# Kernel optimization log

Hardware: AMD Instinct MI355X
Metric: run time of the kernel (lower is better)

## Reference

```python
import jax, jax.numpy as jnp
import numpy as np
import math

B, P = 64, 2048
E_DRUG, E_PATH = 512, 512
ATTN_DIM, H, DEPTH = 1024, 8, 1
HD = ATTN_DIM // (2 * H)          # head_dim = 64
SCALING = HD ** (-0.5)
LAMBDA_INIT = 0.8 - 0.6 * math.exp(-0.3 * DEPTH)
EPS_SM = 1e-20
EPS_RMS = 1e-5


def stable_softmax(x, eps=EPS_SM):
    x = x.astype(jnp.float32)
    x = x - jnp.max(x, axis=-1, keepdims=True)
    ex = jnp.exp(x)
    return ex / (jnp.sum(ex, axis=-1, keepdims=True) + eps)


def setup_inputs() -> dict:
    key = jax.random.key(0)
    ks = jax.random.split(key, 11)
    d = 2 * H * HD  # = ATTN_DIM
    return {
        "query": jax.random.normal(ks[0], (B, 1, E_DRUG), jnp.float32),
        "key": jax.random.normal(ks[1], (B, P, E_PATH), jnp.float32),
        # Linear weights stored [in, out] (transpose of torch storage; same math)
        "Wq": jax.random.normal(ks[2], (E_DRUG, d), jnp.float32) * 0.02,
        "Wk": jax.random.normal(ks[3], (E_PATH, d), jnp.float32) * 0.02,
        "Wv": jax.random.normal(ks[4], (E_PATH, d), jnp.float32) * 0.02,
        "Wo": jax.random.normal(ks[5], (d, E_DRUG), jnp.float32) * 0.02,
        "lambda_q1": jax.random.normal(ks[6], (HD,), jnp.float32) * 0.1,
        "lambda_k1": jax.random.normal(ks[7], (HD,), jnp.float32) * 0.1,
        "lambda_q2": jax.random.normal(ks[8], (HD,), jnp.float32) * 0.1,
        "lambda_k2": jax.random.normal(ks[9], (HD,), jnp.float32) * 0.1,
        "rms_weight": jnp.ones((2 * HD,), jnp.float32),
    }


def reference(query, key, Wq, Wk, Wv, Wo,
              lambda_q1, lambda_k1, lambda_q2, lambda_k2, rms_weight):
    # Q: [B,1,H,2,HD] -> [B,H,2,1,HD]; K,V: [B,P,H,2,HD] -> [B,H,2,P,HD]
    Q = (query @ Wq).reshape(B, 1, H, 2, HD).transpose(0, 2, 3, 1, 4) * SCALING
    K = (key @ Wk).reshape(B, P, H, 2, HD).transpose(0, 2, 3, 1, 4)
    V = (key @ Wv).reshape(B, P, H, 2, HD)

    # scores: [B,H,2,1,P]
    scores = jnp.einsum('bhsqd,bhskd->bhsqk', Q, K)
    scores = stable_softmax(scores)

    lam1 = jnp.exp(jnp.sum(lambda_q1 * lambda_k1))
    lam2 = jnp.exp(jnp.sum(lambda_q2 * lambda_k2))
    lam = lam1 - lam2 + LAMBDA_INIT

    diff_attn = scores[:, :, 0] - lam * scores[:, :, 1]  # [B,H,1,P]

    V_cat = V.transpose(0, 2, 1, 3, 4).reshape(B, H, P, 2 * HD)  # [B,H,P,2HD]
    out = jnp.einsum('bhqp,bhpd->bhqd', diff_attn, V_cat)        # [B,H,1,2HD]

    # RMSNorm over last dim, affine
    var = jnp.mean(out * out, axis=-1, keepdims=True)
    out = out * jax.lax.rsqrt(var + EPS_RMS) * rms_weight
    out = out * (1.0 - LAMBDA_INIT)

    out = out.transpose(0, 2, 1, 3).reshape(B, 1, 2 * H * HD)
    out = out @ Wo  # [B,1,E_DRUG]
    return out, diff_attn
```

## Files before the change

### kernel.cpp

```cpp
#include <hip/hip_runtime.h>
#include <hip/hip_bf16.h>
#include <math.h>

#define B_ 64
#define P_ 2048
#define E_ 512
#define H_ 8
#define D_ 1024
#define NC_ 32
#define NG_ 4
#define SMEM_FUSED (65536 + 8704 + 2304 + 64 + 64)

#define BAR() do { __builtin_amdgcn_sched_barrier(0); \
                   asm volatile("s_waitcnt lgkmcnt(0)"); \
                   __builtin_amdgcn_s_barrier(); \
                   __builtin_amdgcn_sched_barrier(0); } while (0)

#define KXOR(row) ((((row) & 7) << 3) ^ (((row) & 8) << 1) ^ (((row) & 16) >> 1))

static constexpr float SCALING_C = 0.125f;
static constexpr float LAMBDA_INIT_C = 0.35550906759096966f;

typedef float f32x4 __attribute__((ext_vector_type(4)));
typedef float f32x2 __attribute__((ext_vector_type(2)));
typedef short bf16x8 __attribute__((ext_vector_type(8)));
typedef short bf16x4 __attribute__((ext_vector_type(4)));

static __device__ __forceinline__ short f2bf(float f) {
    __hip_bfloat16 h = __float2bfloat16(f);
    return __builtin_bit_cast(short, h);
}

__global__ __launch_bounds__(256) void k_qproj(const float* __restrict__ query,
                                               const float* __restrict__ Wq,
                                               const float* __restrict__ Wk,
                                               unsigned short* __restrict__ qkfrag) {
    int x = blockIdx.x, b = blockIdx.y, t = threadIdx.x;
    __shared__ float q[E_];
    __shared__ float qh[256];
    q[t] = query[b * E_ + t];
    q[t + 256] = query[b * E_ + t + 256];
    __syncthreads();
    {
        int j = x * 256 + t;
        const float* w = Wq + j;
        float s[8] = {0.f,0.f,0.f,0.f,0.f,0.f,0.f,0.f};
        #pragma unroll 4
        for (int e = 0; e < E_; e += 8) {
            #pragma unroll
            for (int k = 0; k < 8; ++k) s[k] += q[e + k] * w[(long)(e + k) * D_];
        }
        qh[t] = (((s[0]+s[1])+(s[2]+s[3])) + ((s[4]+s[5])+(s[6]+s[7]))) * SCALING_C;
    }
    __syncthreads();
    int hs_loc = t >> 6, l = t & 63;
    int hs = x * 4 + hs_loc;
    int e0 = l * 8;
    const float* qp = qh + hs_loc * 64;
    float acc[8];
    #pragma unroll
    for (int jj = 0; jj < 8; ++jj) {
        const f32x4* w = (const f32x4*)(Wk + (long)(e0 + jj) * D_ + hs * 64);
        float s = 0.f;
        #pragma unroll
        for (int d4 = 0; d4 < 16; ++d4) {
            f32x4 wv = w[d4];
            s += qp[d4 * 4 + 0] * wv[0] + qp[d4 * 4 + 1] * wv[1]
               + qp[d4 * 4 + 2] * wv[2] + qp[d4 * 4 + 3] * wv[3];
        }
        acc[jj] = s;
    }
    bf16x8 v;
    #pragma unroll
    for (int jj = 0; jj < 8; ++jj) v[jj] = f2bf(acc[jj]);
    *(bf16x8*)(qkfrag + (((long)b * 16 + (l >> 2)) * 64 + (l & 3) * 16 + hs) * 8) = v;
}

__global__ __launch_bounds__(512, 2) void k_fusedp(const float* __restrict__ key,
                                                   const unsigned short* __restrict__ qkfrag,
                                                   float* __restrict__ wexp,
                                                   float* __restrict__ ms, float* __restrict__ zs,
                                                   float* __restrict__ apart) {
    extern __shared__ __align__(16) char smem[];
    unsigned short* kswz = (unsigned short*)smem;
    float* scr           = (float*)(smem + 65536);
    unsigned short* wbf  = (unsigned short*)(smem + 74240);
    float* fac_l         = (float*)(smem + 76544);
    float* mrun_l        = (float*)(smem + 76608);

    int pcg = blockIdx.x, b = blockIdx.y;
    int t = threadIdx.x, wv = t >> 6, l = t & 63;
    int rt = wv >> 1, eh = wv & 1;
    int prow = rt * 16 + (l & 15);
    int xorv = KXOR(prow);
    int hi = t >> 7;
    int col4 = t & 127;

    if (t < 16) mrun_l[t] = -3.0e38f;

    bf16x8 qfr[8];
    {
        const bf16x8* qf = (const bf16x8*)(qkfrag + (long)b * 16 * 64 * 8);
        #pragma unroll
        for (int s = 0; s < 8; ++s) qfr[s] = qf[(eh * 8 + s) * 64 + l];
    }

    const float* kchunk = key + ((long)b * P_ + pcg * 512) * E_;

    f32x4 x[16];
    #pragma unroll
    for (int r = 0; r < 16; ++r)
        x[r] = *(const f32x4*)(kchunk + (long)(r * 512 + t) * 4);

    f32x4 accp[4];
    #pragma unroll
    for (int i = 0; i < 4; ++i) accp[i] = {0.f, 0.f, 0.f, 0.f};

    for (int c = 0; c < 8; ++c) {
        #pragma unroll
        for (int r = 0; r < 16; ++r) {
            int row = 4 * r + hi;
            int xr = KXOR(row);
            bf16x4 wb;
            wb[0] = f2bf(x[r][0]); wb[1] = f2bf(x[r][1]);
            wb[2] = f2bf(x[r][2]); wb[3] = f2bf(x[r][3]);
            *(bf16x4*)(kswz + row * 512 + ((col4 * 4) ^ xr)) = wb;
        }
        if (c < 7) {
            const float* kn = kchunk + (long)(c + 1) * 64 * E_;
            #pragma unroll
            for (int r = 0; r < 16; ++r)
                x[r] = *(const f32x4*)(kn + (long)(r * 512 + t) * 4);
        }
        BAR();

        {
            f32x4 acc = {0.f, 0.f, 0.f, 0.f};
            #pragma unroll
            for (int s = 0; s < 8; ++s) {
                int e8 = eh * 256 + (l >> 4) * 8 + s * 32;
                bf16x8 a = *(const bf16x8*)(kswz + prow * 512 + (e8 ^ xorv));
                acc = __builtin_amdgcn_mfma_f32_16x16x32_bf16(a, qfr[s], acc, 0, 0, 0);
            }
            #pragma unroll
            for (int r = 0; r < 4; ++r)
                scr[eh * 1088 + (l & 15) * 68 + rt * 16 + (l >> 4) * 4 + r] = acc[r];
        }
        BAR();

        {
            int hs = t >> 5, i = t & 31;
            const float* s0p = scr + hs * 68 + i * 2;
            const float* s1p = s0p + 1088;
            float v0 = s0p[0] + s1p[0];
            float v1 = s0p[1] + s1p[1];
            float m = fmaxf(v0, v1);
            #pragma unroll
            for (int o = 16; o > 0; o >>= 1) m = fmaxf(m, __shfl_xor(m, o));
            float e0v = expf(v0 - m), e1v = expf(v1 - m);
            float z = e0v + e1v;
            #pragma unroll
            for (int o = 16; o > 0; o >>= 1) z += __shfl_xor(z, o);
            float mold = mrun_l[hs];
            float mnew = fmaxf(mold, m);
            float wsc = expf(m - mnew);
            if (i == 0) {
                mrun_l[hs] = mnew;
                fac_l[hs] = expf(mold - mnew);
                ms[((long)(pcg * 8 + c) * B_ + b) * 16 + hs] = m;
                zs[((long)(pcg * 8 + c) * B_ + b) * 16 + hs] = z;
            }
            f32x2 wv2; wv2[0] = e0v; wv2[1] = e1v;
            *(f32x2*)(wexp + ((long)b * 16 + hs) * P_ + pcg * 512 + c * 64 + i * 2) = wv2;
            unsigned lo = (unsigned short)f2bf(e0v * wsc);
            unsigned hi2 = (unsigned short)f2bf(e1v * wsc);
            *(unsigned*)(wbf + hs * 72 + i * 2) = lo | (hi2 << 16);
        }
        BAR();

        {
            f32x4 frv;
            frv[0] = fac_l[(l >> 4) * 4 + 0];
            frv[1] = fac_l[(l >> 4) * 4 + 1];
            frv[2] = fac_l[(l >> 4) * 4 + 2];
            frv[3] = fac_l[(l >> 4) * 4 + 3];
            const unsigned short* wrow = wbf + (l & 15) * 72;
            bf16x8 af0 = *(const bf16x8*)(wrow + (l >> 4) * 8);
            bf16x8 af1 = *(const bf16x8*)(wrow + 32 + (l >> 4) * 8);
            #pragma unroll
            for (int tile = 0; tile < 4; ++tile) {
                accp[tile] = accp[tile] * frv;
                int e = wv * 64 + tile * 16 + (l & 15);
                #pragma unroll
                for (int ks = 0; ks < 2; ++ks) {
                    int pbase = ks * 32 + (l >> 4) * 8;
                    bf16x8 af = ks ? af1 : af0;
                    int xc = ((pbase & 8) << 1) ^ ((pbase & 16) >> 1);
                    bf16x8 bfv;
                    #pragma unroll
                    for (int j = 0; j < 8; ++j)
                        bfv[j] = (short)kswz[(pbase + j) * 512 + (e ^ (j << 3) ^ xc)];
                    accp[tile] = __builtin_amdgcn_mfma_f32_16x16x32_bf16(af, bfv, accp[tile], 0, 0, 0);
                }
            }
        }
        BAR();
    }

    {
        long abase = ((long)pcg * B_ + b) * 16 * E_;
        #pragma unroll
        for (int tile = 0; tile < 4; ++tile) {
            int e = wv * 64 + tile * 16 + (l & 15);
            #pragma unroll
            for (int r = 0; r < 4; ++r)
                apart[abase + (long)((l >> 4) * 4 + r) * E_ + e] = accp[tile][r];
        }
    }
}

__global__ __launch_bounds__(256) void k_comb(const float* __restrict__ wexp,
                                              const float* __restrict__ ms, const float* __restrict__ zs,
                                              const float* __restrict__ apart,
                                              const float* __restrict__ lq1, const float* __restrict__ lk1,
                                              const float* __restrict__ lq2, const float* __restrict__ lk2,
                                              const float* __restrict__ Wv, const float* __restrict__ rmsw,
                                              float* __restrict__ out1, float* __restrict__ on) {
    int h = blockIdx.x, b = blockIdx.y, t = threadIdx.x;
    __shared__ float lam_s;
    __shared__ float mc0s[NC_], mc1s[NC_], zc0s[NC_], zc1s[NC_];
    __shared__ float c0s[NC_], c1s[NC_];
    __shared__ float attk[E_];
    __shared__ float onred[2][128];
    __shared__ float red[4];
    int hs0 = 2 * h, hs1 = 2 * h + 1;
    if (t < 64) {
        float v1 = lq1[t] * lk1[t];
        float v2 = lq2[t] * lk2[t];
        #pragma unroll
        for (int o = 32; o > 0; o >>= 1) { v1 += __shfl_xor(v1, o); v2 += __shfl_xor(v2, o); }
        if (t == 0) lam_s = expf(v1) - expf(v2) + LAMBDA_INIT_C;
    }
    if (t >= 64 && t < 64 + NC_) {
        int c = t - 64;
        mc0s[c] = ms[((long)c * B_ + b) * 16 + hs0];
        mc1s[c] = ms[((long)c * B_ + b) * 16 + hs1];
        zc0s[c] = zs[((long)c * B_ + b) * 16 + hs0];
        zc1s[c] = zs[((long)c * B_ + b) * 16 + hs1];
    }
    __syncthreads();
    float m0 = -3.0e38f, m1 = -3.0e38f;
    #pragma unroll
    for (int c = 0; c < NC_; ++c) { m0 = fmaxf(m0, mc0s[c]); m1 = fmaxf(m1, mc1s[c]); }
    float z0 = 0.f, z1 = 0.f;
    #pragma unroll
    for (int c = 0; c < NC_; ++c) {
        z0 += zc0s[c] * expf(mc0s[c] - m0);
        z1 += zc1s[c] * expf(mc1s[c] - m1);
    }
    float lam = lam_s;
    float i0 = 1.f / (z0 + 1e-20f);
    float i1 = lam / (z1 + 1e-20f);
    if (t < NC_) {
        c0s[t] = expf(mc0s[t] - m0) * i0;
        c1s[t] = expf(mc1s[t] - m1) * i1;
    }
    __syncthreads();
    const float* w0p = wexp + ((long)b * 16 + hs0) * P_;
    const float* w1p = wexp + ((long)b * 16 + hs1) * P_;
    float* dst = out1 + ((long)b * H_ + h) * P_;
    #pragma unroll
    for (int c8 = 0; c8 < 8; ++c8) {
        int p = c8 * 256 + t;
        dst[p] = w0p[p] * c0s[p >> 6] - w1p[p] * c1s[p >> 6];
    }
    float cg0[NG_], cg1[NG_];
    #pragma unroll
    for (int g = 0; g < NG_; ++g) {
        float mg0 = -3.0e38f, mg1 = -3.0e38f;
        #pragma unroll
        for (int q = 0; q < 8; ++q) {
            mg0 = fmaxf(mg0, mc0s[g * 8 + q]);
            mg1 = fmaxf(mg1, mc1s[g * 8 + q]);
        }
        cg0[g] = expf(mg0 - m0) * i0;
        cg1[g] = expf(mg1 - m1) * i1;
    }
    #pragma unroll
    for (int k = 0; k < 2; ++k) {
        int e = k * 256 + t;
        float s = 0.f;
        #pragma unroll
        for (int g = 0; g < NG_; ++g) {
            s += cg0[g] * apart[(((long)g * B_ + b) * 16 + hs0) * E_ + e]
               - cg1[g] * apart[(((long)g * B_ + b) * 16 + hs1) * E_ + e];
        }
        attk[e] = s;
    }
    __syncthreads();
    int j = t & 127, half = t >> 7;
    const float* w = Wv + (long)(half * 256) * D_ + h * 128 + j;
    const float* aa = attk + half * 256;
    float s[8] = {0.f,0.f,0.f,0.f,0.f,0.f,0.f,0.f};
    #pragma unroll 4
    for (int e = 0; e < 256; e += 8) {
        #pragma unroll
        for (int k = 0; k < 8; ++k) s[k] += aa[e + k] * w[(long)(e + k) * D_];
    }
    onred[half][j] = ((s[0]+s[1])+(s[2]+s[3])) + ((s[4]+s[5])+(s[6]+s[7]));
    __syncthreads();
    float v = 0.f;
    if (t < 128) v = onred[0][t] + onred[1][t];
    float sq = v * v;
    int wv2 = t >> 6, ln = t & 63;
    #pragma unroll
    for (int o = 32; o > 0; o >>= 1) sq += __shfl_xor(sq, o);
    if (ln == 0) red[wv2] = sq;
    __syncthreads();
    float tot = red[0] + red[1];
    float scale = rsqrtf(tot * (1.f / 128.f) + 1e-5f) * (1.f - LAMBDA_INIT_C);
    if (t < 128) on[(long)b * D_ + h * 128 + t] = v * scale * rmsw[t];
}

__global__ __launch_bounds__(256) void k_wo(const float* __restrict__ on,
                                            const float* __restrict__ Wo,
                                            float* __restrict__ wop) {
    int kc = blockIdx.x >> 1, oc = blockIdx.x & 1, b = blockIdx.y;
    int t = threadIdx.x;
    __shared__ float sh[256];
    sh[t] = on[(long)b * D_ + kc * 256 + t];
    __syncthreads();
    int o = oc * 256 + t;
    const float* w = Wo + (long)(kc * 256) * 512 + o;
    float s[8] = {0.f,0.f,0.f,0.f,0.f,0.f,0.f,0.f};
    #pragma unroll 4
    for (int k = 0; k < 256; k += 8) {
        #pragma unroll
        for (int q = 0; q < 8; ++q) s[q] += sh[k + q] * w[(long)(k + q) * 512];
    }
    wop[((long)kc * B_ + b) * 512 + o] = ((s[0]+s[1])+(s[2]+s[3])) + ((s[4]+s[5])+(s[6]+s[7]));
}

__global__ __launch_bounds__(256) void k_wored(const float* __restrict__ wop,
                                               float* __restrict__ out0) {
    int b = blockIdx.x, t = threadIdx.x;
    #pragma unroll
    for (int i = 0; i < 2; ++i) {
        int o = i * 256 + t;
        float s = 0.f;
        #pragma unroll
        for (int kc = 0; kc < 4; ++kc) s += wop[((long)kc * B_ + b) * 512 + o];
        out0[(long)b * 512 + o] = s;
    }
}

extern "C" void kernel_launch(void* const* d_in, const int* in_sizes, int n_in,
                              void* d_out, int out_size, void* d_ws, size_t ws_size,
                              hipStream_t stream) {
    const float* query = (const float*)d_in[0];
    const float* key   = (const float*)d_in[1];
    const float* Wq    = (const float*)d_in[2];
    const float* Wk    = (const float*)d_in[3];
    const float* Wv    = (const float*)d_in[4];
    const float* Wo    = (const float*)d_in[5];
    const float* lq1   = (const float*)d_in[6];
    const float* lk1   = (const float*)d_in[7];
    const float* lq2   = (const float*)d_in[8];
    const float* lk2   = (const float*)d_in[9];
    const float* rmsw  = (const float*)d_in[10];

    float* out0 = (float*)d_out;
    float* out1 = out0 + B_ * E_;

    unsigned short* qkfrag = (unsigned short*)d_ws;
    float* wexp  = (float*)d_ws + 262144;
    float* apart = wexp + (long)B_ * 16 * P_;
    float* ms    = apart + (long)NG_ * B_ * 16 * E_;
    float* zs    = ms + NC_ * B_ * 16;
    float* on    = zs + NC_ * B_ * 16;
    float* wop   = on + B_ * D_;

    hipFuncSetAttribute((const void*)k_fusedp,
                        hipFuncAttributeMaxDynamicSharedMemorySize, SMEM_FUSED);

    hipLaunchKernelGGL(k_qproj,  dim3(4, B_),   dim3(256), 0, stream, query, Wq, Wk, qkfrag);
    hipLaunchKernelGGL(k_fusedp, dim3(NG_, B_), dim3(512), SMEM_FUSED, stream,
                       key, qkfrag, wexp, ms, zs, apart);
    hipLaunchKernelGGL(k_comb,   dim3(H_, B_),  dim3(256), 0, stream, wexp, ms, zs, apart,
                       lq1, lk1, lq2, lk2, Wv, rmsw, out1, on);
    hipLaunchKernelGGL(k_wo,     dim3(8, B_),   dim3(256), 0, stream, on, Wo, wop);
    hipLaunchKernelGGL(k_wored,  dim3(B_),      dim3(256), 0, stream, wop, out0);
}
```

Before: 119.5 us.

## Double-buffer K tile in LDS and store softmax exponentials as bf16

The fused projection kernel now alternates between two 64KB LDS buffers for the bf16 K tile. This lets it drop the trailing barrier at the end of each chunk iteration. The unnormalized exponentials written to workspace are packed as bf16 instead of fp32, which halves that intermediate write and the matching read in the combine kernel. LDS per block grows to about 142KB, and the attention output now carries bf16 rounding of the exponentials, which could affect accuracy tolerance.

```diff
diff --git a/kernel.cpp b/kernel.cpp
--- a/kernel.cpp
+++ b/kernel.cpp
@@ -9,7 +9,7 @@
 #define D_ 1024
 #define NC_ 32
 #define NG_ 4
-#define SMEM_FUSED (65536 + 8704 + 2304 + 64 + 64)
+#define SMEM_FUSED (131072 + 8704 + 2304 + 64 + 64)
 
 #define BAR() do { __builtin_amdgcn_sched_barrier(0); \
                    asm volatile("s_waitcnt lgkmcnt(0)"); \
@@ -29,6 +29,9 @@
 static __device__ __forceinline__ short f2bf(float f) {
     __hip_bfloat16 h = __float2bfloat16(f);
     return __builtin_bit_cast(short, h);
+}
+static __device__ __forceinline__ float bf2f(unsigned short s) {
+    return __builtin_bit_cast(float, (unsigned)s << 16);
 }
 
 __global__ __launch_bounds__(256) void k_qproj(const float* __restrict__ query,
@@ -78,15 +81,14 @@
 
 __global__ __launch_bounds__(512, 2) void k_fusedp(const float* __restrict__ key,
                                                    const unsigned short* __restrict__ qkfrag,
-                                                   float* __restrict__ wexp,
+                                                   unsigned short* __restrict__ wexp,
                                                    float* __restrict__ ms, float* __restrict__ zs,
                                                    float* __restrict__ apart) {
     extern __shared__ __align__(16) char smem[];
-    unsigned short* kswz = (unsigned short*)smem;
-    float* scr           = (float*)(smem + 65536);
-    unsigned short* wbf  = (unsigned short*)(smem + 74240);
-    float* fac_l         = (float*)(smem + 76544);
-    float* mrun_l        = (float*)(smem + 76608);
+    float* scr           = (float*)(smem + 131072);
+    unsigned short* wbf  = (unsigned short*)(smem + 139776);
+    float* fac_l         = (float*)(smem + 142080);
+    float* mrun_l        = (float*)(smem + 142144);
 
     int pcg = blockIdx.x, b = blockIdx.y;
     int t = threadIdx.x, wv = t >> 6, l = t & 63;
@@ -117,6 +119,7 @@
     for (int i = 0; i < 4; ++i) accp[i] = {0.f, 0.f, 0.f, 0.f};
 
     for (int c = 0; c < 8; ++c) {
+        unsigned short* kz = (unsigned short*)(smem + (c & 1) * 65536);
         #pragma unroll
         for (int r = 0; r < 16; ++r) {
             int row = 4 * r + hi;
@@ -124,7 +127,7 @@
             bf16x4 wb;
             wb[0] = f2bf(x[r][0]); wb[1] = f2bf(x[r][1]);
             wb[2] = f2bf(x[r][2]); wb[3] = f2bf(x[r][3]);
-            *(bf16x4*)(kswz + row * 512 + ((col4 * 4) ^ xr)) = wb;
+            *(bf16x4*)(kz + row * 512 + ((col4 * 4) ^ xr)) = wb;
         }
         if (c < 7) {
             const float* kn = kchunk + (long)(c + 1) * 64 * E_;
@@ -139,7 +142,7 @@
             #pragma unroll
             for (int s = 0; s < 8; ++s) {
                 int e8 = eh * 256 + (l >> 4) * 8 + s * 32;
-                bf16x8 a = *(const bf16x8*)(kswz + prow * 512 + (e8 ^ xorv));
+                bf16x8 a = *(const bf16x8*)(kz + prow * 512 + (e8 ^ xorv));
                 acc = __builtin_amdgcn_mfma_f32_16x16x32_bf16(a, qfr[s], acc, 0, 0, 0);
             }
             #pragma unroll
@@ -170,8 +173,9 @@
                 ms[((long)(pcg * 8 + c) * B_ + b) * 16 + hs] = m;
                 zs[((long)(pcg * 8 + c) * B_ + b) * 16 + hs] = z;
             }
-            f32x2 wv2; wv2[0] = e0v; wv2[1] = e1v;
-            *(f32x2*)(wexp + ((long)b * 16 + hs) * P_ + pcg * 512 + c * 64 + i * 2) = wv2;
+            unsigned wpack = (unsigned)(unsigned short)f2bf(e0v)
+                           | ((unsigned)(unsigned short)f2bf(e1v) << 16);
+            *(unsigned*)(wexp + ((long)b * 16 + hs) * P_ + pcg * 512 + c * 64 + i * 2) = wpack;
             unsigned lo = (unsigned short)f2bf(e0v * wsc);
             unsigned hi2 = (unsigned short)f2bf(e1v * wsc);
             *(unsigned*)(wbf + hs * 72 + i * 2) = lo | (hi2 << 16);
@@ -199,12 +203,11 @@
                     bf16x8 bfv;
                     #pragma unroll
                     for (int j = 0; j < 8; ++j)
-                        bfv[j] = (short)kswz[(pbase + j) * 512 + (e ^ (j << 3) ^ xc)];
+                        bfv[j] = (short)kz[(pbase + j) * 512 + (e ^ (j << 3) ^ xc)];
                     accp[tile] = __builtin_amdgcn_mfma_f32_16x16x32_bf16(af, bfv, accp[tile], 0, 0, 0);
                 }
             }
         }
-        BAR();
     }
 
     {
@@ -219,7 +222,7 @@
     }
 }
 
-__global__ __launch_bounds__(256) void k_comb(const float* __restrict__ wexp,
+__global__ __launch_bounds__(256) void k_comb(const unsigned short* __restrict__ wexp,
                                               const float* __restrict__ ms, const float* __restrict__ zs,
                                               const float* __restrict__ apart,
                                               const float* __restrict__ lq1, const float* __restrict__ lk1,
@@ -266,13 +269,18 @@
         c1s[t] = expf(mc1s[t] - m1) * i1;
     }
     __syncthreads();
-    const float* w0p = wexp + ((long)b * 16 + hs0) * P_;
-    const float* w1p = wexp + ((long)b * 16 + hs1) * P_;
+    const unsigned* w0p = (const unsigned*)(wexp + ((long)b * 16 + hs0) * P_);
+    const unsigned* w1p = (const unsigned*)(wexp + ((long)b * 16 + hs1) * P_);
     float* dst = out1 + ((long)b * H_ + h) * P_;
     #pragma unroll
-    for (int c8 = 0; c8 < 8; ++c8) {
-        int p = c8 * 256 + t;
-        dst[p] = w0p[p] * c0s[p >> 6] - w1p[p] * c1s[p >> 6];
+    for (int k4 = 0; k4 < 4; ++k4) {
+        int idx = k4 * 256 + t;
+        unsigned w0 = w0p[idx], w1 = w1p[idx];
+        int p0 = idx * 2;
+        int cc = p0 >> 6;
+        dst[p0]     = bf2f((unsigned short)w0) * c0s[cc] - bf2f((unsigned short)w1) * c1s[cc];
+        dst[p0 + 1] = bf2f((unsigned short)(w0 >> 16)) * c0s[cc]
+                    - bf2f((unsigned short)(w1 >> 16)) * c1s[cc];
     }
     float cg0[NG_], cg1[NG_];
     #pragma unroll
@@ -373,8 +381,8 @@
     float* out1 = out0 + B_ * E_;
 
     unsigned short* qkfrag = (unsigned short*)d_ws;
-    float* wexp  = (float*)d_ws + 262144;
-    float* apart = wexp + (long)B_ * 16 * P_;
+    unsigned short* wexp = (unsigned short*)((float*)d_ws + 262144);
+    float* apart = (float*)d_ws + 262144 + 1048576;
     float* ms    = apart + (long)NG_ * B_ * 16 * E_;
     float* zs    = ms + NC_ * B_ * 16;
     float* on    = zs + NC_ * B_ * 16;
```

Result: no change. 117.8 us (-1.4%).
